# Optimization experiments

Measured on AMD Instinct MI355X. Metric: run time of the kernel, lower is better.

## Reference

```python
import jax, jax.numpy as jnp
import numpy as np

EPS_NORM = 1e-5   # instance-norm epsilon (NormalizeLayer over spatial axes)
EPS_VAR = 1e-9    # floor used before sqrt, as in the original


def _instance_norm(x):
    # normalize over spatial axes (1,2), per batch & channel
    mean = jnp.mean(x, axis=(1, 2), keepdims=True)
    var = jnp.var(x, axis=(1, 2), keepdims=True)
    return (x - mean) * jax.lax.rsqrt(var + EPS_NORM)


def _aat(content, style, comb_c, comb_s):
    # content/style: (B,H,W,C); comb_*: (B,H,W,Cc)
    B, H, W, C = content.shape
    N = H * W
    norm_content = _instance_norm(content)
    q = _instance_norm(comb_c).reshape(B, N, -1)   # (B,N,Cc)
    k = _instance_norm(comb_s).reshape(B, N, -1)   # (B,N,Cc)
    v = style.reshape(B, N, C)                     # (B,N,C)
    scores = jnp.einsum('bnc,bmc->bnm', q, k)      # Q_T @ K
    A = jax.nn.softmax(scores, axis=-1)            # (B,N,N)
    M = jnp.einsum('bnm,bmc->bnc', A, v)           # weighted mean
    S2 = jnp.einsum('bnm,bmc->bnc', A, v * v) - M * M  # weighted variance
    S = jnp.sqrt(jnp.maximum(jax.nn.relu(S2), EPS_VAR))
    S = S.reshape(B, H, W, C)
    M = M.reshape(B, H, W, C)
    return S * norm_content + M


def _feature_loss(cs, c, s, cc, sc):
    aat = _aat(c, s, cc, sc)
    return jnp.mean(jnp.square(cs - aat))


def setup_inputs() -> dict:
    key = jax.random.key(0)
    shapes = {
        'cs2': (4, 64, 64, 256), 'c2': (4, 64, 64, 256), 's2': (4, 64, 64, 256),
        'cc2': (4, 64, 64, 448), 'sc2': (4, 64, 64, 448),
        'cs3': (4, 32, 32, 512), 'c3': (4, 32, 32, 512), 's3': (4, 32, 32, 512),
        'cc3': (4, 32, 32, 960), 'sc3': (4, 32, 32, 960),
        'cs4': (4, 16, 16, 512), 'c4': (4, 16, 16, 512), 's4': (4, 16, 16, 512),
        'cc4': (4, 16, 16, 1472), 'sc4': (4, 16, 16, 1472),
    }
    keys = jax.random.split(key, len(shapes))
    return {name: jax.random.normal(k, shp, dtype=jnp.float32)
            for k, (name, shp) in zip(keys, shapes.items())}


def reference(cs2, c2, s2, cc2, sc2, cs3, c3, s3, cc3, sc3, cs4, c4, s4, cc4, sc4):
    loss = _feature_loss(cs2, c2, s2, cc2, sc2)
    loss = loss + _feature_loss(cs3, c3, s3, cc3, sc3)
    loss = loss + _feature_loss(cs4, c4, s4, cc4, sc4)
    return loss
```

## Files before the change

### kernel.cpp

```cpp
#include <hip/hip_runtime.h>
#include <math.h>

#define EPS_NORM 1e-5f
#define EPS_VAR  1e-9f
#define LOG2E    1.4426950408889634f

typedef unsigned short ushort_t;
typedef __attribute__((ext_vector_type(4))) float f32x4;
typedef _Float16 half8 __attribute__((ext_vector_type(8)));

#define MFMAH(a, b, c) __builtin_amdgcn_mfma_f32_16x16x32_f16((a), (b), (c), 0, 0, 0)

#define GLD16(gp, lp) __builtin_amdgcn_global_load_lds(                          \
    (const __attribute__((address_space(1))) unsigned int*)(gp),                 \
    (__attribute__((address_space(3))) unsigned int*)(lp), 16, 0, 0)

__device__ inline ushort_t f16_bits(float x) {
    _Float16 h = (_Float16)x;
    ushort_t u;
    __builtin_memcpy(&u, &h, 2);
    return u;
}
__device__ inline half8 ldh(const ushort_t* p) {
    half8 h;
// ... 13 lines not shown
    const float* x[9];
    float* sm[9];
    float* sq[9];
    int N[9], Cn[9], chG[9], nG[9], base[9];
};
__global__ void __launch_bounds__(256) stat_partial_all(StatJobs J)
{
    int bx = blockIdx.x;
    int j = 0;
#pragma unroll
    for (int k = 1; k < 9; ++k) if (bx >= J.base[k]) j = k;
    bx -= J.base[j];
    const int N = J.N[j], Cn = J.Cn[j], chG = J.chG[j], nG = J.nG[j];
    int b  = bx / (chG * nG);
    int r  = bx % (chG * nG);
    int cg = r / nG;
    int ng = r % nG;
    int ch = cg * 256 + threadIdx.x;
    if (ch >= Cn) return;
    int n0 = ng * 256;
    int n1 = min(n0 + 256, N);
    const float* p = J.x[j] + (long)(b * N) * Cn + ch;
    float s = 0.f, ss = 0.f;
    for (int n = n0; n < n1; ++n) {
        float v = p[(long)n * Cn];
        s += v;
        ss = fmaf(v, v, ss);
    }
    atomicAdd(&J.sm[j][b * Cn + ch], s);
    atomicAdd(&J.sq[j][b * Cn + ch], ss);
}

struct FinJobs {
    float* sm[9];
    float* sq[9];
    int base[9];
    float invN[9];
    int total;
};
__global__ void __launch_bounds__(256) stat_finalize_all(FinJobs J)
{
    int i = blockIdx.x * 256 + threadIdx.x;
    if (i >= J.total) return;
    int j = 0;
#pragma unroll
    for (int k = 1; k < 9; ++k) if (i >= J.base[k]) j = k;
    int e = i - J.base[j];
    float m = J.sm[j][e] * J.invN[j];
    float v = J.sq[j][e] * J.invN[j] - m * m;
    J.sm[j][e] = m;
    J.sq[j][e] = rsqrtf(v + EPS_NORM);
}

__global__ void __launch_bounds__(256) prep_scale(
    const float* __restrict__ qx, const float* __restrict__ qm, const float* __restrict__ qr,
    ushort_t* __restrict__ qh,
    const float* __restrict__ kx, const float* __restrict__ km, const float* __restrict__ kr,
    ushort_t* __restrict__ kh,
    const float* __restrict__ vx, ushort_t* __restrict__ vt,
    int N, int Cc, int C, int KSEG)
{
    const int R = 4 * N;
    int bid = blockIdx.x;
    if (bid < 2 * R) {
        const bool isQ = bid < R;
        int bn = isQ ? bid : bid - R;
        const float* x    = isQ ? qx : kx;
        const float* mean = isQ ? qm : km;
        const float* rstd = isQ ? qr : kr;
        ushort_t* out     = isQ ? qh : kh;
        const float scl   = isQ ? LOG2E : 1.0f;
        int b = bn / N;
        long base = (long)bn * Cc;
        for (int ch = threadIdx.x; ch < Cc; ch += 256) {
            float v = (x[base + ch] - mean[b * Cc + ch]) * rstd[b * Cc + ch] * scl;
            out[base + ch] = f16_bits(v);
        }
    } else {
        int bid2 = bid - 2 * R;
        int cPB = C / 64, nSeg = N / KSEG;
        int b   = bid2 / (cPB * nSeg);
        int rem = bid2 % (cPB * nSeg);
        int cb  = rem / nSeg;
        int ns  = rem % nSeg;
        int ch  = cb * 64 + (threadIdx.x & 63);
        const int KL = KSEG / 4;
        int k0  = ns * KSEG + (threadIdx.x >> 6) * KL;
        long obase = ((long)b * C + ch) * N;
        for (int k = k0; k < k0 + KL; k += 8) {
            ushort_t h8[8];
#pragma unroll
            for (int i = 0; i < 8; ++i)
                h8[i] = f16_bits(vx[((long)b * N + k + i) * C + ch]);
            *(uint4*)(vt + obase + k) = pack8(h8);
        }
    }
}

__device__ inline void stage64_async(const ushort_t* __restrict__ g, long rowBase,
                                     int gstride, int col0, ushort_t* slab, int tid)
{
    const int l  = tid & 63, w = tid >> 6;
    const int rs = l >> 3;
    const int cg = (l & 7) ^ rs;
#pragma unroll
    for (int i = 0; i < 2; ++i) {
        const int r = w * 16 + i * 8 + rs;
        const ushort_t* gp = g + (rowBase + r) * (long)gstride + col0 + (cg << 3);
        ushort_t* lp = slab + (w * 16 + i * 8) * 64 + l * 8;
        GLD16(gp, lp);
    }
}
template<int BROWS>
__device__ inline void stageQ_async(const ushort_t* __restrict__ g, long rowBase,
                                    int gstride, int col0, ushort_t* slab, int tid)
{
    if (tid < BROWS * 8) {
        const int l  = tid & 63, w = tid >> 6;
        const int rs = l >> 3;
        const int cg = (l & 7) ^ rs;
        const int r  = w * 8 + rs;
        const ushort_t* gp = g + (rowBase + r) * (long)gstride + col0 + (cg << 3);
        ushort_t* lp = slab + w * 8 * 64 + l * 8;
        GLD16(gp, lp);
    }
}
__device__ inline half8 ldsw(const ushort_t* slab, int row, int soff)
{
    const int gr = (soff >> 3) ^ (row & 7);
    return ldh(slab + row * 64 + (gr << 3));
}

__global__ void __launch_bounds__(256, 2) flash_pipe(
    const ushort_t* __restrict__ Qh, const ushort_t* __restrict__ Kh,
    const ushort_t* __restrict__ Vth,
    float* __restrict__ Pmo, float* __restrict__ Plo,
    float* __restrict__ PMo, float* __restrict__ PSo)
{
    constexpr int Cc = 448, C = 256, N = 4096, SPLIT = 2;
    constexpr int NKT  = (N / 64) / SPLIT;
    constexpr long VCHO = 64L * N;
    constexpr long KADV = 64L * Cc;

    __shared__ __align__(16) ushort_t smem[2 * 16384 + 4 * 1152];
    const int tid  = threadIdx.x;
    const int lane = tid & 63;
    const int w    = tid >> 6;
    const int l15  = lane & 15;
    const int quad = lane >> 4;

    const int bq = blockIdx.x / SPLIT;
    const int sp = blockIdx.x % SPLIT;
    const int b  = bq / (N / 64);
    const int qb = bq % (N / 64);
    const int i0 = qb * 64 + w * 16;
    const long po = (long)(b * (N / 16) + qb * 4 + w) * SPLIT + sp;

    const int rs    = lane >> 3;
    const int cg    = (lane & 7) ^ rs;
    const int ldso0 = w * 1024 + lane * 8;
    const int ldso1 = ldso0 + 512;
    const int xh    = l15 & 7;
    const int lb0   = l15 * 64 + ((quad)     ^ xh) * 8;
    const int lb1   = l15 * 64 + ((4 + quad) ^ xh) * 8;
    ushort_t* const Pw  = smem + 32768 + w * 1152;
    ushort_t* const pww = Pw + quad * 288 + l15;
    const ushort_t* const pfr = Pw + l15 * 72 + quad * 8;

    const long krow0 = (long)b * N + (long)sp * NKT * 64;
    const ushort_t* kp0 = Kh + (krow0 + w * 16 + rs) * (long)Cc + (cg << 3);
    const ushort_t* kp1 = kp0 + 8 * Cc;
    const ushort_t* vp0 = Vth + ((long)b * C + w * 16 + rs) * (long)N
                              + (cg << 3) + (long)sp * NKT * 64;
    const ushort_t* vp1 = vp0 + 8 * (long)N;

#define STGK(c, dst) do { GLD16(kp0 + (c) * 64, (dst) + ldso0);                  \
                          GLD16(kp1 + (c) * 64, (dst) + ldso1); } while (0)
#define STGV(c, dst) do { GLD16(vp0 + (c) * VCHO, (dst) + ldso0);                \
                          GLD16(vp1 + (c) * VCHO, (dst) + ldso1); } while (0)

    half8 qf[14];
    {
        const ushort_t* q1 = Qh + ((long)(b * N + i0 + l15)) * Cc + quad * 8;
#pragma unroll
        for (int ks = 0; ks < 14; ++ks) qf[ks] = ldh(q1 + ks * 32);
    }

    float m_r[4], l_l[4], mw = -1e30f;
    f32x4 Mac[16], Sac[16];
#pragma unroll
    for (int r = 0; r < 4; ++r) { m_r[r] = -1e30f; l_l[r] = 0.f; }
#pragma unroll
    for (int ct = 0; ct < 16; ++ct)
#pragma unroll
        for (int r = 0; r < 4; ++r) { Mac[ct][r] = 0.f; Sac[ct][r] = 0.f; }

    STGK(0, smem + 0);
    STGK(1, smem + 4096);
    STGK(2, smem + 8192);
    STGK(3, smem + 12288);
    int cur = 0;

    for (int t = 0; t < NKT; ++t) {
        f32x4 S[4];
#pragma unroll
        for (int ct = 0; ct < 4; ++ct)
#pragma unroll
            for (int r = 0; r < 4; ++r) S[ct][r] = 0.f;

        ushort_t* bufc = smem + cur * 16384;
        ushort_t* bufo = smem + (cur ^ 1) * 16384;

        __builtin_amdgcn_s_barrier();
        STGK(4, bufo + 0);
        STGK(5, bufo + 4096);
        STGK(6, bufo + 8192);
        asm volatile("s_waitcnt vmcnt(6)" ::: "memory");
        __builtin_amdgcn_sched_barrier(0);
        __builtin_amdgcn_s_barrier();
        __builtin_amdgcn_s_setprio(1);
#pragma unroll
        for (int j = 0; j < 4; ++j) {
            const ushort_t* sl = bufc + j * 4096;
#pragma unroll
            for (int ct = 0; ct < 4; ++ct) S[ct] = MFMAH(qf[j * 2 + 0], ldh(sl + ct * 1024 + lb0), S[ct]);
#pragma unroll
            for (int ct = 0; ct < 4; ++ct) S[ct] = MFMAH(qf[j * 2 + 1], ldh(sl + ct * 1024 + lb1), S[ct]);
        }
        __builtin_amdgcn_s_setprio(0);
        cur ^= 1; bufc = smem + cur * 16384; bufo = smem + (cur ^ 1) * 16384;

        __builtin_amdgcn_s_barrier();
        STGV(0, bufo + 0);
        STGV(1, bufo + 4096);
        STGV(2, bufo + 8192);
        STGV(3, bufo + 12288);
        asm volatile("s_waitcnt vmcnt(8)" ::: "memory");
        __builtin_amdgcn_sched_barrier(0);
        __builtin_amdgcn_s_barrier();
        __builtin_amdgcn_s_setprio(1);
#pragma unroll
        for (int j = 0; j < 3; ++j) {
            const ushort_t* sl = bufc + j * 4096;
#pragma unroll
            for (int ct = 0; ct < 4; ++ct) S[ct] = MFMAH(qf[(4 + j) * 2 + 0], ldh(sl + ct * 1024 + lb0), S[ct]);
#pragma unroll
            for (int ct = 0; ct < 4; ++ct) S[ct] = MFMAH(qf[(4 + j) * 2 + 1], ldh(sl + ct * 1024 + lb1), S[ct]);
        }
        __builtin_amdgcn_s_setprio(0);

        {
            float tmax = S[0][0];
#pragma unroll
            for (int ct = 0; ct < 4; ++ct)
#pragma unroll
                for (int r = 0; r < 4; ++r) tmax = fmaxf(tmax, S[ct][r]);
#pragma unroll
            for (int off = 1; off <= 32; off <<= 1)
                tmax = fmaxf(tmax, __shfl_xor(tmax, off, 64));

            if (tmax > mw + 14.4269504f) {
                float rm[4];
#pragma unroll
                for (int r = 0; r < 4; ++r)
                    rm[r] = fmaxf(fmaxf(S[0][r], S[1][r]), fmaxf(S[2][r], S[3][r]));
#pragma unroll
                for (int off = 1; off <= 8; off <<= 1)
#pragma unroll
                    for (int r = 0; r < 4; ++r)
                        rm[r] = fmaxf(rm[r], __shfl_xor(rm[r], off, 64));
#pragma unroll
                for (int r = 0; r < 4; ++r) {
                    float mn = fmaxf(m_r[r], rm[r]);
                    float corr = exp2f(m_r[r] - mn);
                    m_r[r] = mn;
                    l_l[r] *= corr;
#pragma unroll
                    for (int ct = 0; ct < 16; ++ct) { Mac[ct][r] *= corr; Sac[ct][r] *= corr; }
                }
                float tt = fminf(fminf(m_r[0], m_r[1]), fminf(m_r[2], m_r[3]));
                tt = fminf(tt, __shfl_xor(tt, 16, 64));
                tt = fminf(tt, __shfl_xor(tt, 32, 64));
                mw = tt;
            }

#pragma unroll
            for (int ct = 0; ct < 4; ++ct)
#pragma unroll
                for (int r = 0; r < 4; ++r) {
                    float p = exp2f(S[ct][r] - m_r[r]);
                    l_l[r] += p;
                    pww[r * 72 + ct * 16] = f16_bits(p);
                }
        }
        half8 pf0 = ldh(pfr);
        half8 pf1 = ldh(pfr + 32);
        cur ^= 1; bufc = smem + cur * 16384; bufo = smem + (cur ^ 1) * 16384;

        __builtin_amdgcn_s_barrier();
        if (t + 1 < NKT) {
            kp0 += KADV; kp1 += KADV;
            STGK(0, bufo + 0);
            STGK(1, bufo + 4096);
            STGK(2, bufo + 8192);
            STGK(3, bufo + 12288);
            asm volatile("s_waitcnt vmcnt(8)" ::: "memory");
        } else {
            asm volatile("s_waitcnt vmcnt(0)" ::: "memory");
        }
        __builtin_amdgcn_sched_barrier(0);
        __builtin_amdgcn_s_barrier();
        __builtin_amdgcn_s_setprio(1);
#define PVSLAB(J) do {                                                           \
        const ushort_t* sl = bufc + (J) * 4096;                                  \
        _Pragma("unroll")                                                        \
        for (int ct = 0; ct < 4; ++ct) {                                         \
            half8 vh = ldh(sl + ct * 1024 + lb0);                                \
            half8 uh = vh * vh;                                                  \
            Mac[(J) * 4 + ct] = MFMAH(pf0, vh, Mac[(J) * 4 + ct]);               \
            Sac[(J) * 4 + ct] = MFMAH(pf0, uh, Sac[(J) * 4 + ct]);               \
        }                                                                        \
        _Pragma("unroll")                                                        \
        for (int ct = 0; ct < 4; ++ct) {                                         \
            half8 vh = ldh(sl + ct * 1024 + lb1);                                \
            half8 uh = vh * vh;                                                  \
            Mac[(J) * 4 + ct] = MFMAH(pf1, vh, Mac[(J) * 4 + ct]);               \
            Sac[(J) * 4 + ct] = MFMAH(pf1, uh, Sac[(J) * 4 + ct]);               \
        } } while (0)
        PVSLAB(0); PVSLAB(1); PVSLAB(2); PVSLAB(3);
#undef PVSLAB
        __builtin_amdgcn_s_setprio(0);
        cur ^= 1;
        vp0 += 64; vp1 += 64;
    }
#undef STGK
#undef STGV

#pragma unroll
    for (int off = 1; off <= 8; off <<= 1)
#pragma unroll
        for (int r = 0; r < 4; ++r) l_l[r] += __shfl_xor(l_l[r], off, 64);

    if (l15 == 0) {
#pragma unroll
        for (int r = 0; r < 4; ++r) {
            Pmo[po * 16 + quad * 4 + r] = m_r[r];
            Plo[po * 16 + quad * 4 + r] = l_l[r];
        }
    }
#pragma unroll
    for (int ct = 0; ct < 16; ++ct)
#pragma unroll
        for (int r = 0; r < 4; ++r) {
            long idx = (po * 16 + quad * 4 + r) * C + ct * 16 + l15;
            PMo[idx] = Mac[ct][r];
            PSo[idx] = Sac[ct][r];
        }
}

template<int Cc, int C, int N, int CSPLIT, bool QREG, int SPLIT, int SLABS, int KGRP>
__global__ void __launch_bounds__(256, 2) flash_mfma(
    const ushort_t* __restrict__ Qh, const ushort_t* __restrict__ Kh,
    const ushort_t* __restrict__ Vth,
    float* __restrict__ Pmo, float* __restrict__ Plo,
    float* __restrict__ PMo, float* __restrict__ PSo)
{
    constexpr int KC      = Cc / 64;
    constexpr int VC      = C / 64;
    constexpr int VCW     = VC / CSPLIT;
    constexpr int CTCW    = 4 * VCW;
    constexpr int STRIPES = 4 / CSPLIT;
    constexpr int BROWS   = 16 * STRIPES;
    constexpr int QB      = N / BROWS;
    constexpr int TILES   = N / 64;
    constexpr int NKT     = TILES / SPLIT;
    constexpr int NKS     = QREG ? (Cc / 32) : 1;
    constexpr int NGRP    = (KC + KGRP - 1) / KGRP;
    constexpr int G       = 4 / CSPLIT;
    constexpr int QCH     = BROWS * 64;
    constexpr int QOFF    = KGRP * 4096;
    constexpr int KQEND   = QOFF + KGRP * QCH;
    constexpr int REGION  = QREG ? (SLABS * 4096)
                                 : (KQEND > SLABS * 4096 ? KQEND : SLABS * 4096);

    __shared__ __align__(16) ushort_t smem[REGION + 4 * 1152];
    const int tid  = threadIdx.x;
    const int lane = tid & 63;
    const int w    = tid >> 6;
    const int l15  = lane & 15;
// ... 118 lines not shown
                stage64_async(Vth, (long)b * C + (h * VCW + g + j) * 64, N, kt * 64,
                              smem + s * 4096, tid);
            }
            __syncthreads();
#pragma unroll
            for (int ks = 0; ks < 2; ++ks) {
                half8 pf = ks ? pf1 : pf0;
#pragma unroll
                for (int j = 0; j < G; ++j)
#pragma unroll
                    for (int ct = 0; ct < 4; ++ct) {
                        half8 vh = ldsw(smem + (ch2 * G + j) * 4096,
                                        ct * 16 + l15, ks * 32 + quad * 8);
                        half8 uh = vh * vh;
                        const int ci = (g + j) * 4 + ct;
                        Mac[ci] = MFMAH(pf, vh, Mac[ci]);
                        Sac[ci] = MFMAH(pf, uh, Sac[ci]);
                    }
            }
        }
    }

#pragma unroll
    for (int off = 1; off <= 8; off <<= 1)
#pragma unroll
        for (int r = 0; r < 4; ++r) l_l[r] += __shfl_xor(l_l[r], off, 64);

    if (ch2 == 0 && l15 == 0) {
#pragma unroll
        for (int r = 0; r < 4; ++r) {
            Pmo[po * 16 + quad * 4 + r] = m_r[r];
            Plo[po * 16 + quad * 4 + r] = l_l[r];
        }
    }
    const int chb = ch2 * (C / CSPLIT);
#pragma unroll
    for (int ct = 0; ct < CTCW; ++ct)
#pragma unroll
        for (int r = 0; r < 4; ++r) {
            long idx = (po * 16 + quad * 4 + r) * C + chb + ct * 16 + l15;
            PMo[idx] = Mac[ct][r];
            PSo[idx] = Sac[ct][r];
        }
}

template<int C, int SPLIT>
__global__ void __launch_bounds__(256) combine_aat(
    const float* __restrict__ Pm, const float* __restrict__ Pl,
    const float* __restrict__ PM, const float* __restrict__ PS,
    const float* __restrict__ CT, const float* __restrict__ CS,
    const float* __restrict__ cmean, const float* __restrict__ crstd,
    float* __restrict__ loss, int N)
{
    __shared__ float wS[SPLIT][16];
    __shared__ float invL[16];
    __shared__ float red[4];
    const int pi = blockIdx.x;
    const int nb = N / 16;
    const int b  = pi / nb;
    const long g0 = (long)b * N + (long)(pi % nb) * 16;
    const int tid = threadIdx.x;

    if (tid < 16) {
        float m = -1e30f;
#pragma unroll
        for (int s = 0; s < SPLIT; ++s)
            m = fmaxf(m, Pm[((long)pi * SPLIT + s) * 16 + tid]);
        float L = 0.f;
#pragma unroll
        for (int s = 0; s < SPLIT; ++s) {
            float e = exp2f(Pm[((long)pi * SPLIT + s) * 16 + tid] - m);
            wS[s][tid] = e;
            L = fmaf(e, Pl[((long)pi * SPLIT + s) * 16 + tid], L);
        }
        invL[tid] = 1.f / L;
    }
    __syncthreads();

    float acc = 0.f;
    for (int e = tid; e < 16 * C; e += 256) {
        const int r  = e / C;
        const int ch = e % C;
        float Ms = 0.f, Ss = 0.f;
#pragma unroll
        for (int s = 0; s < SPLIT; ++s) {
            const long q = (((long)pi * SPLIT + s) * 16 + r) * C + ch;
            Ms = fmaf(wS[s][r], PM[q], Ms);
            Ss = fmaf(wS[s][r], PS[q], Ss);
        }
        const float M  = Ms * invL[r];
        const float S2 = Ss * invL[r] - M * M;
        const float S  = sqrtf(fmaxf(S2, EPS_VAR));
        const float nc = (CT[(g0 + r) * C + ch] - cmean[b * C + ch]) * crstd[b * C + ch];
        const float d  = CS[(g0 + r) * C + ch] - (S * nc + M);
        acc = fmaf(d, d, acc);
    }
#pragma unroll
    for (int off = 1; off <= 32; off <<= 1) acc += __shfl_xor(acc, off, 64);
    if ((tid & 63) == 0) red[tid >> 6] = acc;
    __syncthreads();
    if (tid == 0) atomicAdd(loss, red[0] + red[1] + red[2] + red[3]);
}

template<int CCL, int CL, int NQ>
__global__ void __launch_bounds__(256) flash_aat(
    const float* __restrict__ Q, const float* __restrict__ K, const float* __restrict__ V,
    const float* __restrict__ CT, const float* __restrict__ CS,
    const float* __restrict__ qmean, const float* __restrict__ qrstd,
    const float* __restrict__ kmean, const float* __restrict__ krstd,
    const float* __restrict__ cmean, const float* __restrict__ crstd,
    float* __restrict__ loss, int N)
{
    constexpr int CC   = CCL * 64;
    constexpr int C    = CL * 64;
    constexpr int ROWS = 4 * NQ;
    const int lane = threadIdx.x & 63;
    const int wave = threadIdx.x >> 6;
    const int rowBlocks = N / ROWS;
    const int b  = blockIdx.x / rowBlocks;
    const int rb = blockIdx.x % rowBlocks;
    const int i0 = rb * ROWS + wave * NQ;

    float kmu[CCL], krs[CCL];
#pragma unroll
    for (int t = 0; t < CCL; ++t) {
        int ch = lane + 64 * t;
        kmu[t] = kmean[b * CC + ch];
        krs[t] = krstd[b * CC + ch];
    }
    float q[NQ][CCL];
#pragma unroll
    for (int qi = 0; qi < NQ; ++qi) {
        long base = (long)(b * N + i0 + qi) * CC;
#pragma unroll
        for (int t = 0; t < CCL; ++t) {
            int ch = lane + 64 * t;
            q[qi][t] = (Q[base + ch] - qmean[b * CC + ch]) * qrstd[b * CC + ch];
        }
    }
    float mval[NQ], lsum[NQ];
    float Macc[NQ][CL], Sacc[NQ][CL];
#pragma unroll
    for (int qi = 0; qi < NQ; ++qi) {
        mval[qi] = -1e30f; lsum[qi] = 0.f;
#pragma unroll
        for (int t = 0; t < CL; ++t) { Macc[qi][t] = 0.f; Sacc[qi][t] = 0.f; }
    }
    for (int j = 0; j < N; ++j) {
// ... 87 lines not shown
    size_t fo = 0;
    auto allocF = [&](size_t n) { float* p = ws + fo; fo += n; return p; };

    float* lossp = allocF(4);
    float* c2m = allocF(B * 256);  float* c2r = allocF(B * 256);
    float* q2m = allocF(B * 448);  float* q2r = allocF(B * 448);
    float* k2m = allocF(B * 448);  float* k2r = allocF(B * 448);
    float* c3m = allocF(B * 512);  float* c3r = allocF(B * 512);
    float* q3m = allocF(B * 960);  float* q3r = allocF(B * 960);
    float* k3m = allocF(B * 960);  float* k3r = allocF(B * 960);
    float* c4m = allocF(B * 512);  float* c4r = allocF(B * 512);
    float* q4m = allocF(B * 1472); float* q4r = allocF(B * 1472);
    float* k4m = allocF(B * 1472); float* k4r = allocF(B * 1472);
    size_t zeroBytes = fo * sizeof(float);

    float* Pm = allocF(32768);
    float* Pl = allocF(32768);
    float* PM = allocF(8388608);
    float* PS = allocF(8388608);

    size_t arenaOff = ((fo * 4 + 15) & ~(size_t)15) / 2;
    ushort_t* arena = (ushort_t*)d_ws + arenaOff;
    const size_t arenaShorts = 18874400;
    size_t need = arenaOff * 2 + arenaShorts * 2;
    const bool fast = (ws_size >= need);

    hipMemsetAsync(d_ws, 0, zeroBytes, stream);

    {
        StatJobs SJ; FinJobs FJ;
        const float* xs[9] = {c2, cc2, sc2, c3, cc3, sc3, c4, cc4, sc4};
        float* sms[9] = {c2m, q2m, k2m, c3m, q3m, k3m, c4m, q4m, k4m};
        float* sqs[9] = {c2r, q2r, k2r, c3r, q3r, k3r, c4r, q4r, k4r};
        const int Ns[9]  = {4096, 4096, 4096, 1024, 1024, 1024, 256, 256, 256};
        const int Cns[9] = {256, 448, 448, 512, 960, 960, 512, 1472, 1472};
        int pb = 0, fb = 0;
        for (int j = 0; j < 9; ++j) {
            int chG = (Cns[j] + 255) / 256;
            int nG  = (Ns[j] + 255) / 256;
            SJ.x[j] = xs[j]; SJ.sm[j] = sms[j]; SJ.sq[j] = sqs[j];
            SJ.N[j] = Ns[j]; SJ.Cn[j] = Cns[j]; SJ.chG[j] = chG; SJ.nG[j] = nG;
            SJ.base[j] = pb;
            pb += B * chG * nG;
            FJ.sm[j] = sms[j]; FJ.sq[j] = sqs[j]; FJ.base[j] = fb;
            FJ.invN[j] = 1.0f / (float)Ns[j];
            fb += B * Cns[j];
        }
        FJ.total = fb;
        hipLaunchKernelGGL(stat_partial_all, dim3(pb), dim3(256), 0, stream, SJ);
        hipLaunchKernelGGL(stat_finalize_all, dim3((fb + 255) / 256), dim3(256), 0, stream, FJ);
    }

    if (fast) {
        {
            size_t o = 0;
            auto aU = [&](size_t n) { ushort_t* p = arena + o; o += (n + 7) & ~(size_t)7; return p; };
            ushort_t *qh = aU((size_t)B*4096*448), *kh = aU((size_t)B*4096*448);
            ushort_t *vh = aU((size_t)B*4096*256);
            hipLaunchKernelGGL(prep_scale, dim3(2*B*4096 + B*(256/64)*(4096/512)), dim3(256), 0, stream,
                               cc2, q2m, q2r, qh, sc2, k2m, k2r, kh, s2v, vh, 4096, 448, 256, 512);
            hipLaunchKernelGGL(flash_pipe, dim3(B*(4096/64)*2), dim3(256), 0, stream,
                               qh, kh, vh, Pm, Pl, PM, PS);
            hipLaunchKernelGGL((combine_aat<256, 2>), dim3(B*4096/16), dim3(256), 0, stream,
                               Pm, Pl, PM, PS, c2, cs2, c2m, c2r, &lossp[0], 4096);
        }
        {
            size_t o = 0;
            auto aU = [&](size_t n) { ushort_t* p = arena + o; o += (n + 7) & ~(size_t)7; return p; };
            ushort_t *qh = aU((size_t)B*1024*960), *kh = aU((size_t)B*1024*960);
            ushort_t *vh = aU((size_t)B*1024*512);
            hipLaunchKernelGGL(prep_scale, dim3(2*B*1024 + B*(512/64)*(1024/512)), dim3(256), 0, stream,
                               cc3, q3m, q3r, qh, sc3, k3m, k3r, kh, s3v, vh, 1024, 960, 512, 512);
            hipLaunchKernelGGL((flash_mfma<960, 512, 1024, 2, false, 4, 4, 4>),
                               dim3(B*(1024/32)*4), dim3(256), 0, stream,
                               qh, kh, vh, Pm, Pl, PM, PS);
            hipLaunchKernelGGL((combine_aat<512, 4>), dim3(B*1024/16), dim3(256), 0, stream,
                               Pm, Pl, PM, PS, c3, cs3, c3m, c3r, &lossp[1], 1024);
        }
        {
            size_t o = 0;
            auto aU = [&](size_t n) { ushort_t* p = arena + o; o += (n + 7) & ~(size_t)7; return p; };
            ushort_t *qh = aU((size_t)B*256*1472), *kh = aU((size_t)B*256*1472);
            ushort_t *vh = aU((size_t)B*256*512);
            hipLaunchKernelGGL(prep_scale, dim3(2*B*256 + B*(512/64)*(256/256)), dim3(256), 0, stream,
                               cc4, q4m, q4r, qh, sc4, k4m, k4r, kh, s4v, vh, 256, 1472, 512, 256);
            hipLaunchKernelGGL((flash_mfma<1472, 512, 256, 4, false, 4, 4, 4>),
                               dim3(B*(256/16)*4), dim3(256), 0, stream,
                               qh, kh, vh, Pm, Pl, PM, PS);
            hipLaunchKernelGGL((combine_aat<512, 4>), dim3(B*256/16), dim3(256), 0, stream,
                               Pm, Pl, PM, PS, c4, cs4, c4m, c4r, &lossp[2], 256);
        }
    } else {
        hipLaunchKernelGGL((flash_aat<7, 4, 4>), dim3(B * 4096 / 16), dim3(256), 0, stream,
                           cc2, sc2, s2v, c2, cs2, q2m, q2r, k2m, k2r, c2m, c2r, &lossp[0], 4096);
        hipLaunchKernelGGL((flash_aat<15, 8, 2>), dim3(B * 1024 / 8), dim3(256), 0, stream,
                           cc3, sc3, s3v, c3, cs3, q3m, q3r, k3m, k3r, c3m, c3r, &lossp[1], 1024);
        hipLaunchKernelGGL((flash_aat<23, 8, 2>), dim3(B * 256 / 8), dim3(256), 0, stream,
                           cc4, sc4, s4v, c4, cs4, q4m, q4r, k4m, k4r, c4m, c4r, &lossp[2], 256);
    }

    hipLaunchKernelGGL(combine_loss, dim3(1), dim3(1), 0, stream,
                       lossp, (float*)d_out,
                       1.0f / (4.0f * 4096.0f * 256.0f),
                       1.0f / (4.0f * 1024.0f * 512.0f),
                       1.0f / (4.0f * 256.0f * 512.0f));
}
```

Measured before the change: 751.1 us.

## Fuse prep kernels, vectorize normalization, and restructure flash pipeline into 4-slot ring

Merges the three per-level prep_scale launches into one prep_all launch when workspace allows, with one wave per row and 8-wide vector loads and stores for the normalize-to-fp16 step. Rewrites the flash_pipe main loop to use a four-slot 8K ring buffer with finer-grained staging of K and V pairs, interleaving loads with QK and PV MFMA phases and unrolling two key tiles per iteration. Also changes combine_aat to vectorized float4 processing. These aim to cut launch overhead, memory-access inefficiency, and pipeline bubbles, at the cost of more complex wait-count bookkeeping and a larger workspace requirement for the fused prep path.

```diff
diff --git a/kernel.cpp b/kernel.cpp
--- a/kernel.cpp
+++ b/kernel.cpp
@@ -89,32 +89,60 @@
     J.sq[j][e] = rsqrtf(v + EPS_NORM);
 }
 
-__global__ void __launch_bounds__(256) prep_scale(
-    const float* __restrict__ qx, const float* __restrict__ qm, const float* __restrict__ qr,
-    ushort_t* __restrict__ qh,
-    const float* __restrict__ kx, const float* __restrict__ km, const float* __restrict__ kr,
-    ushort_t* __restrict__ kh,
-    const float* __restrict__ vx, ushort_t* __restrict__ vt,
-    int N, int Cc, int C, int KSEG)
-{
-    const int R = 4 * N;
-    int bid = blockIdx.x;
-    if (bid < 2 * R) {
-        const bool isQ = bid < R;
-        int bn = isQ ? bid : bid - R;
-        const float* x    = isQ ? qx : kx;
-        const float* mean = isQ ? qm : km;
-        const float* rstd = isQ ? qr : kr;
-        ushort_t* out     = isQ ? qh : kh;
+struct PrepJobs {
+    const float* qx[3]; const float* qm[3]; const float* qr[3]; ushort_t* qh[3];
+    const float* kx[3]; const float* km[3]; const float* kr[3]; ushort_t* kh[3];
+    const float* vx[3]; ushort_t* vt[3];
+    int N[3], Cc[3], C[3], KSEG[3], nbase[3];
+};
+__global__ void __launch_bounds__(256) prep_all(PrepJobs J)
+{
+    int bx = blockIdx.x;
+    int j = 0;
+#pragma unroll
+    for (int k = 1; k < 3; ++k) if (bx >= J.nbase[k]) j = k;
+    bx -= J.nbase[j];
+    const int N = J.N[j], Cc = J.Cc[j];
+    const int normBlocks = 2 * N;
+    if (bx < normBlocks) {
+        const int wave = threadIdx.x >> 6, lane = threadIdx.x & 63;
+        int rr = bx * 4 + wave;
+        const int BN = 4 * N;
+        const bool isQ = rr < BN;
+        int bn = isQ ? rr : rr - BN;
+        const float* x    = isQ ? J.qx[j] : J.kx[j];
+        const float* mean = isQ ? J.qm[j] : J.km[j];
+        const float* rstd = isQ ? J.qr[j] : J.kr[j];
+        ushort_t* out     = isQ ? J.qh[j] : J.kh[j];
         const float scl   = isQ ? LOG2E : 1.0f;
         int b = bn / N;
         long base = (long)bn * Cc;
-        for (int ch = threadIdx.x; ch < Cc; ch += 256) {
-            float v = (x[base + ch] - mean[b * Cc + ch]) * rstd[b * Cc + ch] * scl;
-            out[base + ch] = f16_bits(v);
+        const float* mb = mean + b * Cc;
+        const float* rb = rstd + b * Cc;
+        for (int c8 = lane; c8 * 8 < Cc; c8 += 64) {
+            int ch = c8 * 8;
+            float4 a0 = *(const float4*)(x + base + ch);
+            float4 a1 = *(const float4*)(x + base + ch + 4);
+            float4 m0 = *(const float4*)(mb + ch);
+            float4 m1 = *(const float4*)(mb + ch + 4);
+            float4 r0 = *(const float4*)(rb + ch);
+            float4 r1 = *(const float4*)(rb + ch + 4);
+            ushort_t h8[8];
+            h8[0] = f16_bits((a0.x - m0.x) * r0.x * scl);
+            h8[1] = f16_bits((a0.y - m0.y) * r0.y * scl);
+            h8[2] = f16_bits((a0.z - m0.z) * r0.z * scl);
+            h8[3] = f16_bits((a0.w - m0.w) * r0.w * scl);
+            h8[4] = f16_bits((a1.x - m1.x) * r1.x * scl);
+            h8[5] = f16_bits((a1.y - m1.y) * r1.y * scl);
+            h8[6] = f16_bits((a1.z - m1.z) * r1.z * scl);
+            h8[7] = f16_bits((a1.w - m1.w) * r1.w * scl);
+            *(uint4*)(out + base + ch) = pack8(h8);
         }
     } else {
-        int bid2 = bid - 2 * R;
+        int bid2 = bx - normBlocks;
+        const int C = J.C[j], KSEG = J.KSEG[j];
+        const float* vx = J.vx[j];
+        ushort_t* vt = J.vt[j];
         int cPB = C / 64, nSeg = N / KSEG;
         int b   = bid2 / (cPB * nSeg);
         int rem = bid2 % (cPB * nSeg);
@@ -179,7 +207,7 @@
     constexpr long VCHO = 64L * N;
     constexpr long KADV = 64L * Cc;
 
-    __shared__ __align__(16) ushort_t smem[2 * 16384 + 4 * 1152];
+    __shared__ __align__(16) ushort_t smem[4 * 8192 + 4 * 1152];
     const int tid  = threadIdx.x;
     const int lane = tid & 63;
     const int w    = tid >> 6;
@@ -211,10 +239,72 @@
                               + (cg << 3) + (long)sp * NKT * 64;
     const ushort_t* vp1 = vp0 + 8 * (long)N;
 
-#define STGK(c, dst) do { GLD16(kp0 + (c) * 64, (dst) + ldso0);                  \
-                          GLD16(kp1 + (c) * 64, (dst) + ldso1); } while (0)
-#define STGV(c, dst) do { GLD16(vp0 + (c) * VCHO, (dst) + ldso0);                \
-                          GLD16(vp1 + (c) * VCHO, (dst) + ldso1); } while (0)
+#define SLOT(k) (smem + (k) * 8192)
+#define STGKP(c0, c1, slot, toff) do {                                           \
+    GLD16(kp0 + (toff) + (c0) * 64, SLOT(slot) + ldso0);                         \
+    GLD16(kp1 + (toff) + (c0) * 64, SLOT(slot) + ldso1);                         \
+    GLD16(kp0 + (toff) + (c1) * 64, SLOT(slot) + 4096 + ldso0);                  \
+    GLD16(kp1 + (toff) + (c1) * 64, SLOT(slot) + 4096 + ldso1); } while (0)
+#define STGK1(c0, slot, toff) do {                                               \
+    GLD16(kp0 + (toff) + (c0) * 64, SLOT(slot) + ldso0);                         \
+    GLD16(kp1 + (toff) + (c0) * 64, SLOT(slot) + ldso1); } while (0)
+#define STGVP(j0, slot, voff) do {                                               \
+    GLD16(vp0 + (voff) + (j0) * VCHO, SLOT(slot) + ldso0);                       \
+    GLD16(vp1 + (voff) + (j0) * VCHO, SLOT(slot) + ldso1);                       \
+    GLD16(vp0 + (voff) + ((j0) + 1) * VCHO, SLOT(slot) + 4096 + ldso0);          \
+    GLD16(vp1 + (voff) + ((j0) + 1) * VCHO, SLOT(slot) + 4096 + ldso1); } while (0)
+
+#define WAITV(NN) asm volatile("s_waitcnt vmcnt(" #NN ")" ::: "memory");         \
+    __builtin_amdgcn_sched_barrier(0);                                           \
+    __builtin_amdgcn_s_barrier();                                                \
+    __builtin_amdgcn_s_setprio(1);
+#define PH_END __builtin_amdgcn_s_setprio(0);
+
+#define QKPAIR(slot, c0) do {                                                    \
+    const ushort_t* s0_ = SLOT(slot);                                            \
+    const ushort_t* s1_ = s0_ + 4096;                                            \
+    _Pragma("unroll")                                                            \
+    for (int ct = 0; ct < 4; ++ct) S[ct] = MFMAH(qf[2*(c0)+0], ldh(s0_ + ct*1024 + lb0), S[ct]); \
+    _Pragma("unroll")                                                            \
+    for (int ct = 0; ct < 4; ++ct) S[ct] = MFMAH(qf[2*(c0)+1], ldh(s0_ + ct*1024 + lb1), S[ct]); \
+    _Pragma("unroll")                                                            \
+    for (int ct = 0; ct < 4; ++ct) S[ct] = MFMAH(qf[2*(c0)+2], ldh(s1_ + ct*1024 + lb0), S[ct]); \
+    _Pragma("unroll")                                                            \
+    for (int ct = 0; ct < 4; ++ct) S[ct] = MFMAH(qf[2*(c0)+3], ldh(s1_ + ct*1024 + lb1), S[ct]); } while (0)
+#define QK1(slot, c0) do {                                                       \
+    const ushort_t* s0_ = SLOT(slot);                                            \
+    _Pragma("unroll")                                                            \
+    for (int ct = 0; ct < 4; ++ct) S[ct] = MFMAH(qf[2*(c0)+0], ldh(s0_ + ct*1024 + lb0), S[ct]); \
+    _Pragma("unroll")                                                            \
+    for (int ct = 0; ct < 4; ++ct) S[ct] = MFMAH(qf[2*(c0)+1], ldh(s0_ + ct*1024 + lb1), S[ct]); } while (0)
+#define PVPAIR(slot, ci0) do {                                                   \
+    const ushort_t* s0_ = SLOT(slot);                                            \
+    const ushort_t* s1_ = s0_ + 4096;                                            \
+    _Pragma("unroll")                                                            \
+    for (int ct = 0; ct < 4; ++ct) {                                             \
+        half8 vh = ldh(s0_ + ct*1024 + lb0); half8 uh = vh * vh;                 \
+        Mac[(ci0)*4 + ct] = MFMAH(pf0, vh, Mac[(ci0)*4 + ct]);                   \
+        Sac[(ci0)*4 + ct] = MFMAH(pf0, uh, Sac[(ci0)*4 + ct]); }                 \
+    _Pragma("unroll")                                                            \
+    for (int ct = 0; ct < 4; ++ct) {                                             \
+        half8 vh = ldh(s0_ + ct*1024 + lb1); half8 uh = vh * vh;                 \
+        Mac[(ci0)*4 + ct] = MFMAH(pf1, vh, Mac[(ci0)*4 + ct]);                   \
+        Sac[(ci0)*4 + ct] = MFMAH(pf1, uh, Sac[(ci0)*4 + ct]); }                 \
+    _Pragma("unroll")                                                            \
+    for (int ct = 0; ct < 4; ++ct) {                                             \
+        half8 vh = ldh(s1_ + ct*1024 + lb0); half8 uh = vh * vh;                 \
+        Mac[(ci0+1)*4 + ct] = MFMAH(pf0, vh, Mac[(ci0+1)*4 + ct]);               \
+        Sac[(ci0+1)*4 + ct] = MFMAH(pf0, uh, Sac[(ci0+1)*4 + ct]); }             \
+    _Pragma("unroll")                                                            \
+    for (int ct = 0; ct < 4; ++ct) {                                             \
+        half8 vh = ldh(s1_ + ct*1024 + lb1); half8 uh = vh * vh;                 \
+        Mac[(ci0+1)*4 + ct] = MFMAH(pf1, vh, Mac[(ci0+1)*4 + ct]);               \
+        Sac[(ci0+1)*4 + ct] = MFMAH(pf1, uh, Sac[(ci0+1)*4 + ct]); } } while (0)
+#define RESET_S do {                                                             \
+    _Pragma("unroll")                                                            \
+    for (int ct = 0; ct < 4; ++ct)                                               \
+        _Pragma("unroll")                                                        \
+        for (int r = 0; r < 4; ++r) S[ct][r] = 0.f; } while (0)
 
     half8 qf[14];
     {
@@ -222,9 +312,12 @@
 #pragma unroll
         for (int ks = 0; ks < 14; ++ks) qf[ks] = ldh(q1 + ks * 32);
     }
+    asm volatile("s_waitcnt vmcnt(0)" ::: "memory");
 
     float m_r[4], l_l[4], mw = -1e30f;
     f32x4 Mac[16], Sac[16];
+    f32x4 S[4];
+    half8 pf0, pf1;
 #pragma unroll
     for (int r = 0; r < 4; ++r) { m_r[r] = -1e30f; l_l[r] = 0.f; }
 #pragma unroll
@@ -232,146 +325,118 @@
 #pragma unroll
         for (int r = 0; r < 4; ++r) { Mac[ct][r] = 0.f; Sac[ct][r] = 0.f; }
 
-    STGK(0, smem + 0);
-    STGK(1, smem + 4096);
-    STGK(2, smem + 8192);
-    STGK(3, smem + 12288);
-    int cur = 0;
-
-    for (int t = 0; t < NKT; ++t) {
-        f32x4 S[4];
+    auto softmax_step = [&]() {
+        float tmax = S[0][0];
 #pragma unroll
         for (int ct = 0; ct < 4; ++ct)
 #pragma unroll
-            for (int r = 0; r < 4; ++r) S[ct][r] = 0.f;
-
-        ushort_t* bufc = smem + cur * 16384;
-        ushort_t* bufo = smem + (cur ^ 1) * 16384;
-
-        __builtin_amdgcn_s_barrier();
-        STGK(4, bufo + 0);
-        STGK(5, bufo + 4096);
-        STGK(6, bufo + 8192);
-        asm volatile("s_waitcnt vmcnt(6)" ::: "memory");
+            for (int r = 0; r < 4; ++r) tmax = fmaxf(tmax, S[ct][r]);
+#pragma unroll
+        for (int off = 1; off <= 32; off <<= 1)
+            tmax = fmaxf(tmax, __shfl_xor(tmax, off, 64));
+
+        if (tmax > mw + 14.4269504f) {
+            float rm[4];
+#pragma unroll
+            for (int r = 0; r < 4; ++r)
+                rm[r] = fmaxf(fmaxf(S[0][r], S[1][r]), fmaxf(S[2][r], S[3][r]));
+#pragma unroll
+            for (int off = 1; off <= 8; off <<= 1)
+#pragma unroll
+                for (int r = 0; r < 4; ++r)
+                    rm[r] = fmaxf(rm[r], __shfl_xor(rm[r], off, 64));
+#pragma unroll
+            for (int r = 0; r < 4; ++r) {
+                float mn = fmaxf(m_r[r], rm[r]);
+                float corr = exp2f(m_r[r] - mn);
+                m_r[r] = mn;
+                l_l[r] *= corr;
+#pragma unroll
+                for (int ct = 0; ct < 16; ++ct) { Mac[ct][r] *= corr; Sac[ct][r] *= corr; }
+            }
+            float tt = fminf(fminf(m_r[0], m_r[1]), fminf(m_r[2], m_r[3]));
+            tt = fminf(tt, __shfl_xor(tt, 16, 64));
+            tt = fminf(tt, __shfl_xor(tt, 32, 64));
+            mw = tt;
+        }
+#pragma unroll
+        for (int ct = 0; ct < 4; ++ct)
+#pragma unroll
+            for (int r = 0; r < 4; ++r) {
+                float p = exp2f(S[ct][r] - m_r[r]);
+                l_l[r] += p;
+                pww[r * 72 + ct * 16] = f16_bits(p);
+            }
+        pf0 = ldh(pfr);
+        pf1 = ldh(pfr + 32);
+    };
+
+    STGKP(0, 1, 0, 0);
+    STGKP(2, 3, 1, 0);
+
+    for (int it = 0; it < NKT / 2; ++it) {
+        RESET_S;
+        STGKP(4, 5, 2, 0);
+        WAITV(8)  QKPAIR(0, 0); PH_END;
+        STGK1(6, 3, 0);
+        WAITV(6)  QKPAIR(1, 2); PH_END;
+        STGVP(0, 0, 0);
+        WAITV(6)  QKPAIR(2, 4); PH_END;
+        STGVP(2, 1, 0);
+        WAITV(8)  QK1(3, 6); PH_END;
+        softmax_step();
+        STGKP(0, 1, 2, KADV);
+        WAITV(8)  PVPAIR(0, 0); PH_END;
+        STGKP(2, 3, 3, KADV);
+        WAITV(8)  PVPAIR(1, 2); PH_END;
+
+        RESET_S;
+        STGKP(4, 5, 0, KADV);
+        WAITV(8)  QKPAIR(2, 0); PH_END;
+        STGK1(6, 1, KADV);
+        WAITV(6)  QKPAIR(3, 2); PH_END;
+        STGVP(0, 2, 64);
+        WAITV(6)  QKPAIR(0, 4); PH_END;
+        STGVP(2, 3, 64);
+        WAITV(8)  QK1(1, 6); PH_END;
+        softmax_step();
+        const bool more = (it + 1 < NKT / 2);
+        if (more) {
+            kp0 += 2 * KADV; kp1 += 2 * KADV;
+            STGKP(0, 1, 0, 0);
+            asm volatile("s_waitcnt vmcnt(8)" ::: "memory");
+        } else {
+            asm volatile("s_waitcnt vmcnt(4)" ::: "memory");
+        }
         __builtin_amdgcn_sched_barrier(0);
         __builtin_amdgcn_s_barrier();
         __builtin_amdgcn_s_setprio(1);
-#pragma unroll
-        for (int j = 0; j < 4; ++j) {
-            const ushort_t* sl = bufc + j * 4096;
-#pragma unroll
-            for (int ct = 0; ct < 4; ++ct) S[ct] = MFMAH(qf[j * 2 + 0], ldh(sl + ct * 1024 + lb0), S[ct]);
-#pragma unroll
-            for (int ct = 0; ct < 4; ++ct) S[ct] = MFMAH(qf[j * 2 + 1], ldh(sl + ct * 1024 + lb1), S[ct]);
-        }
-        __builtin_amdgcn_s_setprio(0);
-        cur ^= 1; bufc = smem + cur * 16384; bufo = smem + (cur ^ 1) * 16384;
-
-        __builtin_amdgcn_s_barrier();
-        STGV(0, bufo + 0);
-        STGV(1, bufo + 4096);
-        STGV(2, bufo + 8192);
-        STGV(3, bufo + 12288);
-        asm volatile("s_waitcnt vmcnt(8)" ::: "memory");
+        PVPAIR(2, 0);
+        PH_END;
+        if (more) {
+            STGKP(2, 3, 1, 0);
+            asm volatile("s_waitcnt vmcnt(8)" ::: "memory");
+        } else {
+            asm volatile("s_waitcnt vmcnt(0)" ::: "memory");
+        }
         __builtin_amdgcn_sched_barrier(0);
         __builtin_amdgcn_s_barrier();
         __builtin_amdgcn_s_setprio(1);
-#pragma unroll
-        for (int j = 0; j < 3; ++j) {
-            const ushort_t* sl = bufc + j * 4096;
-#pragma unroll
-            for (int ct = 0; ct < 4; ++ct) S[ct] = MFMAH(qf[(4 + j) * 2 + 0], ldh(sl + ct * 1024 + lb0), S[ct]);
-#pragma unroll
-            for (int ct = 0; ct < 4; ++ct) S[ct] = MFMAH(qf[(4 + j) * 2 + 1], ldh(sl + ct * 1024 + lb1), S[ct]);
-        }
-        __builtin_amdgcn_s_setprio(0);
-
-        {
-            float tmax = S[0][0];
-#pragma unroll
-            for (int ct = 0; ct < 4; ++ct)
-#pragma unroll
-                for (int r = 0; r < 4; ++r) tmax = fmaxf(tmax, S[ct][r]);
-#pragma unroll
-            for (int off = 1; off <= 32; off <<= 1)
-                tmax = fmaxf(tmax, __shfl_xor(tmax, off, 64));
-
-            if (tmax > mw + 14.4269504f) {
-                float rm[4];
-#pragma unroll
-                for (int r = 0; r < 4; ++r)
-                    rm[r] = fmaxf(fmaxf(S[0][r], S[1][r]), fmaxf(S[2][r], S[3][r]));
-#pragma unroll
-                for (int off = 1; off <= 8; off <<= 1)
-#pragma unroll
-                    for (int r = 0; r < 4; ++r)
-                        rm[r] = fmaxf(rm[r], __shfl_xor(rm[r], off, 64));
-#pragma unroll
-                for (int r = 0; r < 4; ++r) {
-                    float mn = fmaxf(m_r[r], rm[r]);
-                    float corr = exp2f(m_r[r] - mn);
-                    m_r[r] = mn;
-                    l_l[r] *= corr;
-#pragma unroll
-                    for (int ct = 0; ct < 16; ++ct) { Mac[ct][r] *= corr; Sac[ct][r] *= corr; }
-                }
-                float tt = fminf(fminf(m_r[0], m_r[1]), fminf(m_r[2], m_r[3]));
-                tt = fminf(tt, __shfl_xor(tt, 16, 64));
-                tt = fminf(tt, __shfl_xor(tt, 32, 64));
-                mw = tt;
-            }
-
-#pragma unroll
-            for (int ct = 0; ct < 4; ++ct)
-#pragma unroll
-                for (int r = 0; r < 4; ++r) {
-                    float p = exp2f(S[ct][r] - m_r[r]);
-                    l_l[r] += p;
-                    pww[r * 72 + ct * 16] = f16_bits(p);
-                }
-        }
-        half8 pf0 = ldh(pfr);
-        half8 pf1 = ldh(pfr + 32);
-        cur ^= 1; bufc = smem + cur * 16384; bufo = smem + (cur ^ 1) * 16384;
-
-        __builtin_amdgcn_s_barrier();
-        if (t + 1 < NKT) {
-            kp0 += KADV; kp1 += KADV;
-            STGK(0, bufo + 0);
-            STGK(1, bufo + 4096);
-            STGK(2, bufo + 8192);
-            STGK(3, bufo + 12288);
-            asm volatile("s_waitcnt vmcnt(8)" ::: "memory");
-        } else {
-            asm volatile("s_waitcnt vmcnt(0)" ::: "memory");
-        }
-        __builtin_amdgcn_sched_barrier(0);
-        __builtin_amdgcn_s_barrier();
-        __builtin_amdgcn_s_setprio(1);
-#define PVSLAB(J) do {                                                           \
-        const ushort_t* sl = bufc + (J) * 4096;                                  \
-        _Pragma("unroll")                                                        \
-        for (int ct = 0; ct < 4; ++ct) {                                         \
-            half8 vh = ldh(sl + ct * 1024 + lb0);                                \
-            half8 uh = vh * vh;                                                  \
-            Mac[(J) * 4 + ct] = MFMAH(pf0, vh, Mac[(J) * 4 + ct]);               \
-            Sac[(J) * 4 + ct] = MFMAH(pf0, uh, Sac[(J) * 4 + ct]);               \
-        }                                                                        \
-        _Pragma("unroll")                                                        \
-        for (int ct = 0; ct < 4; ++ct) {                                         \
-            half8 vh = ldh(sl + ct * 1024 + lb1);                                \
-            half8 uh = vh * vh;                                                  \
-            Mac[(J) * 4 + ct] = MFMAH(pf1, vh, Mac[(J) * 4 + ct]);               \
-            Sac[(J) * 4 + ct] = MFMAH(pf1, uh, Sac[(J) * 4 + ct]);               \
-        } } while (0)
-        PVSLAB(0); PVSLAB(1); PVSLAB(2); PVSLAB(3);
-#undef PVSLAB
-        __builtin_amdgcn_s_setprio(0);
-        cur ^= 1;
-        vp0 += 64; vp1 += 64;
-    }
-#undef STGK
-#undef STGV
+        PVPAIR(3, 2);
+        PH_END;
+
+        vp0 += 128; vp1 += 128;
+    }
+#undef SLOT
+#undef STGKP
+#undef STGK1
+#undef STGVP
+#undef WAITV
+#undef PH_END
+#undef QKPAIR
+#undef QK1
+#undef PVPAIR
+#undef RESET_S
 
 #pragma unroll
     for (int off = 1; off <= 8; off <<= 1)
@@ -596,6 +661,7 @@
     const float* __restrict__ cmean, const float* __restrict__ crstd,
     float* __restrict__ loss, int N)
 {
+    constexpr int CL4 = C / 4;
     __shared__ float wS[SPLIT][16];
     __shared__ float invL[16];
     __shared__ float red[4];
@@ -622,22 +688,35 @@
     __syncthreads();
 
     float acc = 0.f;
-    for (int e = tid; e < 16 * C; e += 256) {
-        const int r  = e / C;
-        const int ch = e % C;
-        float Ms = 0.f, Ss = 0.f;
+    for (int v = tid; v < 4 * C; v += 256) {
+        const int r  = v / CL4;
+        const int c0 = (v - r * CL4) * 4;
+        const long q0 = (((long)pi * SPLIT) * 16 + r) * C + c0;
+        float4 Ms = {0.f, 0.f, 0.f, 0.f}, Ss = {0.f, 0.f, 0.f, 0.f};
 #pragma unroll
         for (int s = 0; s < SPLIT; ++s) {
-            const long q = (((long)pi * SPLIT + s) * 16 + r) * C + ch;
-            Ms = fmaf(wS[s][r], PM[q], Ms);
-            Ss = fmaf(wS[s][r], PS[q], Ss);
-        }
-        const float M  = Ms * invL[r];
-        const float S2 = Ss * invL[r] - M * M;
-        const float S  = sqrtf(fmaxf(S2, EPS_VAR));
-        const float nc = (CT[(g0 + r) * C + ch] - cmean[b * C + ch]) * crstd[b * C + ch];
-        const float d  = CS[(g0 + r) * C + ch] - (S * nc + M);
-        acc = fmaf(d, d, acc);
+            const float ws_ = wS[s][r];
+            const float4 pm = *(const float4*)&PM[q0 + (long)s * 16 * C];
+            const float4 ps = *(const float4*)&PS[q0 + (long)s * 16 * C];
+            Ms.x = fmaf(ws_, pm.x, Ms.x); Ms.y = fmaf(ws_, pm.y, Ms.y);
+            Ms.z = fmaf(ws_, pm.z, Ms.z); Ms.w = fmaf(ws_, pm.w, Ms.w);
+            Ss.x = fmaf(ws_, ps.x, Ss.x); Ss.y = fmaf(ws_, ps.y, Ss.y);
+            Ss.z = fmaf(ws_, ps.z, Ss.z); Ss.w = fmaf(ws_, ps.w, Ss.w);
+        }
+        const float iL = invL[r];
+        const float4 ctv = *(const float4*)&CT[(g0 + r) * C + c0];
+        const float4 csv = *(const float4*)&CS[(g0 + r) * C + c0];
+        const float4 cmv = *(const float4*)&cmean[b * C + c0];
+        const float4 crv = *(const float4*)&crstd[b * C + c0];
+#pragma unroll
+        for (int e = 0; e < 4; ++e) {
+            const float Msx = (&Ms.x)[e] * iL;
+            const float S2  = (&Ss.x)[e] * iL - Msx * Msx;
+            const float Sx  = sqrtf(fmaxf(S2, EPS_VAR));
+            const float nc  = ((&ctv.x)[e] - (&cmv.x)[e]) * (&crv.x)[e];
+            const float d   = (&csv.x)[e] - (Sx * nc + Msx);
+            acc = fmaf(d, d, acc);
+        }
     }
 #pragma unroll
     for (int off = 1; off <= 32; off <<= 1) acc += __shfl_xor(acc, off, 64);
@@ -831,41 +910,103 @@
     }
 
     if (fast) {
+        auto arenaFor = [&](size_t& o, size_t n) {
+            ushort_t* p = arena + o; o += (n + 7) & ~(size_t)7; return p;
+        };
+        size_t o2 = 0;
+        ushort_t* qh2 = arenaFor(o2, (size_t)B*4096*448);
+        ushort_t* kh2 = arenaFor(o2, (size_t)B*4096*448);
+        ushort_t* vh2 = arenaFor(o2, (size_t)B*4096*256);
+        size_t o3 = 0;
+        ushort_t* qh3 = arenaFor(o3, (size_t)B*1024*960);
+        ushort_t* kh3 = arenaFor(o3, (size_t)B*1024*960);
+        ushort_t* vh3 = arenaFor(o3, (size_t)B*1024*512);
+        size_t o4 = 0;
+        ushort_t* qh4 = arenaFor(o4, (size_t)B*256*1472);
+        ushort_t* kh4 = arenaFor(o4, (size_t)B*256*1472);
+        ushort_t* vh4 = arenaFor(o4, (size_t)B*256*512);
+
+        size_t totShorts = o2 + o3 + o4;
+        bool prepFused = (ws_size >= arenaOff * 2 + totShorts * 2);
+        if (prepFused) {
+            qh3 = arena + o2;        kh3 = qh3 + (((size_t)B*1024*960 + 7) & ~(size_t)7);
+            vh3 = kh3 + (((size_t)B*1024*960 + 7) & ~(size_t)7);
+            qh4 = arena + o2 + o3;   kh4 = qh4 + (((size_t)B*256*1472 + 7) & ~(size_t)7);
+            vh4 = kh4 + (((size_t)B*256*1472 + 7) & ~(size_t)7);
+
+            PrepJobs PJ;
+            PJ.qx[0]=cc2; PJ.qm[0]=q2m; PJ.qr[0]=q2r; PJ.qh[0]=qh2;
+            PJ.kx[0]=sc2; PJ.km[0]=k2m; PJ.kr[0]=k2r; PJ.kh[0]=kh2;
+            PJ.vx[0]=s2v; PJ.vt[0]=vh2; PJ.N[0]=4096; PJ.Cc[0]=448; PJ.C[0]=256; PJ.KSEG[0]=512;
+            PJ.qx[1]=cc3; PJ.qm[1]=q3m; PJ.qr[1]=q3r; PJ.qh[1]=qh3;
+            PJ.kx[1]=sc3; PJ.km[1]=k3m; PJ.kr[1]=k3r; PJ.kh[1]=kh3;
+            PJ.vx[1]=s3v; PJ.vt[1]=vh3; PJ.N[1]=1024; PJ.Cc[1]=960; PJ.C[1]=512; PJ.KSEG[1]=512;
+            PJ.qx[2]=cc4; PJ.qm[2]=q4m; PJ.qr[2]=q4r; PJ.qh[2]=qh4;
+            PJ.kx[2]=sc4; PJ.km[2]=k4m; PJ.kr[2]=k4r; PJ.kh[2]=kh4;
+            PJ.vx[2]=s4v; PJ.vt[2]=vh4; PJ.N[2]=256;  PJ.Cc[2]=1472; PJ.C[2]=512; PJ.KSEG[2]=256;
+            int g0n = 2*4096 + B*(256/64)*(4096/512);
+            int g1n = 2*1024 + B*(512/64)*(1024/512);
+            int g2n = 2*256  + B*(512/64)*(256/256);
+            PJ.nbase[0] = 0; PJ.nbase[1] = g0n; PJ.nbase[2] = g0n + g1n;
+            hipLaunchKernelGGL(prep_all, dim3(g0n + g1n + g2n), dim3(256), 0, stream, PJ);
+        }
+
         {
-            size_t o = 0;
-            auto aU = [&](size_t n) { ushort_t* p = arena + o; o += (n + 7) & ~(size_t)7; return p; };
-            ushort_t *qh = aU((size_t)B*4096*448), *kh = aU((size_t)B*4096*448);
-            ushort_t *vh = aU((size_t)B*4096*256);
-            hipLaunchKernelGGL(prep_scale, dim3(2*B*4096 + B*(256/64)*(4096/512)), dim3(256), 0, stream,
-                               cc2, q2m, q2r, qh, sc2, k2m, k2r, kh, s2v, vh, 4096, 448, 256, 512);
+            if (!prepFused) {
+                PrepJobs PJ;
+                PJ.qx[0]=cc2; PJ.qm[0]=q2m; PJ.qr[0]=q2r; PJ.qh[0]=qh2;
+                PJ.kx[0]=sc2; PJ.km[0]=k2m; PJ.kr[0]=k2r; PJ.kh[0]=kh2;
+                PJ.vx[0]=s2v; PJ.vt[0]=vh2; PJ.N[0]=4096; PJ.Cc[0]=448; PJ.C[0]=256; PJ.KSEG[0]=512;
+                for (int k = 1; k < 3; ++k) { PJ.N[k]=4096; PJ.Cc[k]=448; PJ.C[k]=256; PJ.KSEG[k]=512;
+                    PJ.qx[k]=cc2; PJ.qm[k]=q2m; PJ.qr[k]=q2r; PJ.qh[k]=qh2;
+                    PJ.kx[k]=sc2; PJ.km[k]=k2m; PJ.kr[k]=k2r; PJ.kh[k]=kh2;
+                    PJ.vx[k]=s2v; PJ.vt[k]=vh2; }
+                int gn = 2*4096 + B*(256/64)*(4096/512);
+                PJ.nbase[0]=0; PJ.nbase[1]=gn; PJ.nbase[2]=gn;
+                hipLaunchKernelGGL(prep_all, dim3(gn), dim3(256), 0, stream, PJ);
+            }
             hipLaunchKernelGGL(flash_pipe, dim3(B*(4096/64)*2), dim3(256), 0, stream,
-                               qh, kh, vh, Pm, Pl, PM, PS);
+                               qh2, kh2, vh2, Pm, Pl, PM, PS);
             hipLaunchKernelGGL((combine_aat<256, 2>), dim3(B*4096/16), dim3(256), 0, stream,
                                Pm, Pl, PM, PS, c2, cs2, c2m, c2r, &lossp[0], 4096);
         }
         {
-            size_t o = 0;
-            auto aU = [&](size_t n) { ushort_t* p = arena + o; o += (n + 7) & ~(size_t)7; return p; };
-            ushort_t *qh = aU((size_t)B*1024*960), *kh = aU((size_t)B*1024*960);
-            ushort_t *vh = aU((size_t)B*1024*512);
-            hipLaunchKernelGGL(prep_scale, dim3(2*B*1024 + B*(512/64)*(1024/512)), dim3(256), 0, stream,
-                               cc3, q3m, q3r, qh, sc3, k3m, k3r, kh, s3v, vh, 1024, 960, 512, 512);
+            if (!prepFused) {
+                PrepJobs PJ;
+                PJ.qx[0]=cc3; PJ.qm[0]=q3m; PJ.qr[0]=q3r; PJ.qh[0]=qh3;
+                PJ.kx[0]=sc3; PJ.km[0]=k3m; PJ.kr[0]=k3r; PJ.kh[0]=kh3;
+                PJ.vx[0]=s3v; PJ.vt[0]=vh3; PJ.N[0]=1024; PJ.Cc[0]=960; PJ.C[0]=512; PJ.KSEG[0]=512;
+                for (int k = 1; k < 3; ++k) { PJ.N[k]=1024; PJ.Cc[k]=960; PJ.C[k]=512; PJ.KSEG[k]=512;
+                    PJ.qx[k]=cc3; PJ.qm[k]=q3m; PJ.qr[k]=q3r; PJ.qh[k]=qh3;
+                    PJ.kx[k]=sc3; PJ.km[k]=k3m; PJ.kr[k]=k3r; PJ.kh[k]=kh3;
+                    PJ.vx[k]=s3v; PJ.vt[k]=vh3; }
+                int gn = 2*1024 + B*(512/64)*(1024/512);
+                PJ.nbase[0]=0; PJ.nbase[1]=gn; PJ.nbase[2]=gn;
+                hipLaunchKernelGGL(prep_all, dim3(gn), dim3(256), 0, stream, PJ);
+            }
             hipLaunchKernelGGL((flash_mfma<960, 512, 1024, 2, false, 4, 4, 4>),
                                dim3(B*(1024/32)*4), dim3(256), 0, stream,
-                               qh, kh, vh, Pm, Pl, PM, PS);
+                               qh3, kh3, vh3, Pm, Pl, PM, PS);
             hipLaunchKernelGGL((combine_aat<512, 4>), dim3(B*1024/16), dim3(256), 0, stream,
                                Pm, Pl, PM, PS, c3, cs3, c3m, c3r, &lossp[1], 1024);
         }
         {
-            size_t o = 0;
-            auto aU = [&](size_t n) { ushort_t* p = arena + o; o += (n + 7) & ~(size_t)7; return p; };
-            ushort_t *qh = aU((size_t)B*256*1472), *kh = aU((size_t)B*256*1472);
-            ushort_t *vh = aU((size_t)B*256*512);
-            hipLaunchKernelGGL(prep_scale, dim3(2*B*256 + B*(512/64)*(256/256)), dim3(256), 0, stream,
-                               cc4, q4m, q4r, qh, sc4, k4m, k4r, kh, s4v, vh, 256, 1472, 512, 256);
+            if (!prepFused) {
+                PrepJobs PJ;
+                PJ.qx[0]=cc4; PJ.qm[0]=q4m; PJ.qr[0]=q4r; PJ.qh[0]=qh4;
+                PJ.kx[0]=sc4; PJ.km[0]=k4m; PJ.kr[0]=k4r; PJ.kh[0]=kh4;
+                PJ.vx[0]=s4v; PJ.vt[0]=vh4; PJ.N[0]=256; PJ.Cc[0]=1472; PJ.C[0]=512; PJ.KSEG[0]=256;
+                for (int k = 1; k < 3; ++k) { PJ.N[k]=256; PJ.Cc[k]=1472; PJ.C[k]=512; PJ.KSEG[k]=256;
+                    PJ.qx[k]=cc4; PJ.qm[k]=q4m; PJ.qr[k]=q4r; PJ.qh[k]=qh4;
+                    PJ.kx[k]=sc4; PJ.km[k]=k4m; PJ.kr[k]=k4r; PJ.kh[k]=kh4;
+                    PJ.vx[k]=s4v; PJ.vt[k]=vh4; }
+                int gn = 2*256 + B*(512/64)*(256/256);
+                PJ.nbase[0]=0; PJ.nbase[1]=gn; PJ.nbase[2]=gn;
+                hipLaunchKernelGGL(prep_all, dim3(gn), dim3(256), 0, stream, PJ);
+            }
             hipLaunchKernelGGL((flash_mfma<1472, 512, 256, 4, false, 4, 4, 4>),
                                dim3(B*(256/16)*4), dim3(256), 0, stream,
-                               qh, kh, vh, Pm, Pl, PM, PS);
+                               qh4, kh4, vh4, Pm, Pl, PM, PS);
             hipLaunchKernelGGL((combine_aat<512, 4>), dim3(B*256/16), dim3(256), 0, stream,
                                Pm, Pl, PM, PS, c4, cs4, c4m, c4r, &lossp[2], 256);
         }
```

Measured after the change: 719.2 us. 4.3% less time.
